# Optimization experiments

Hardware: AMD Instinct MI355X
Metric: run time of the kernel (lower is better)

Reference implementation:

```python
import jax, jax.numpy as jnp
import numpy as np

HID = 768        # config.hidden_size
MM_HID = 1024    # config.mmodal_hidden_size
N_Q = 64         # config.num_queries
WIN = 512        # config.window_size
LN_EPS = 1e-5


def _window_starts(m, n, w):
    # mirrors split_tensor's start-index logic (static, computed in numpy)
    step = max(1, (m - w) // (n - 1))
    starts = []
    for i in range(n):
        s = i * step
        if s + w > m:
            s = m - w
        starts.append(s)
    return np.asarray(starts, dtype=np.int32)


def layernorm(x, g, b):
    mu = jnp.mean(x, axis=-1, keepdims=True)
    var = jnp.var(x, axis=-1, keepdims=True)
    return (x - mu) * jax.lax.rsqrt(var + LN_EPS) * g + b


def setup_inputs() -> dict:
    key = jax.random.key(0)
    ks = jax.random.split(key, 12)
    b, m, li = 4, 8192, 77
    s = lambda fan_in: 1.0 / np.sqrt(fan_in)
    inp = {
        'x_mmodal': jax.random.normal(ks[0], (b, m, MM_HID), jnp.float32),
        'inst_feats': jax.random.normal(ks[1], (b, li, HID), jnp.float32),
        'queries': jax.random.normal(ks[2], (1, N_Q, HID), jnp.float32),
        'W_proj': jax.random.normal(ks[3], (HID, HID), jnp.float32) * s(HID),
        'b_proj': jnp.zeros((HID,), jnp.float32),
        'W_kv_inst': jax.random.normal(ks[4], (HID, 2 * HID), jnp.float32) * s(HID),
        'b_kv_inst': jnp.zeros((2 * HID,), jnp.float32),
        'W_out_inst': jax.random.normal(ks[5], (HID, HID), jnp.float32) * s(HID),
        'b_out_inst': jnp.zeros((HID,), jnp.float32),
        'W_kv_mm': jax.random.normal(ks[6], (MM_HID, 2 * HID), jnp.float32) * s(MM_HID),
        'b_kv_mm': jnp.zeros((2 * HID,), jnp.float32),
        'W_out_mm': jax.random.normal(ks[7], (HID, HID), jnp.float32) * s(HID),
        'b_out_mm': jnp.zeros((HID,), jnp.float32),
        'ln_g': jnp.ones((HID,), jnp.float32),
        'ln_b': jnp.zeros((HID,), jnp.float32),
    }
    return inp


def reference(x_mmodal, inst_feats, queries, W_proj, b_proj, W_kv_inst,
              b_kv_inst, W_out_inst, b_out_inst, W_kv_mm, b_kv_mm,
              W_out_mm, b_out_mm, ln_g, ln_b):
    b = x_mmodal.shape[0]
    scale = 1.0 / jnp.sqrt(jnp.asarray(HID, x_mmodal.dtype))

    # ---- dense cross-attention over instruction features ----
    inst = inst_feats @ W_proj + b_proj                      # (b, li, d)
    k, v = jnp.split(inst @ W_kv_inst + b_kv_inst, 2, axis=-1)
    k = layernorm(k, ln_g, ln_b)
    v = layernorm(v, ln_g, ln_b)
    q = jnp.broadcast_to(queries, (b, N_Q, HID))
    attn = jnp.einsum('bnd,bmd->bnm', q, k) * scale
    attn = jax.nn.softmax(attn, axis=-1)
    q = jnp.einsum('bnm,bmd->bnd', attn, v)
    q = layernorm(q @ W_out_inst + b_out_inst, ln_g, ln_b)

    # ---- swin-style overlapping windowed cross-attention over mmodal ----
    k, v = jnp.split(x_mmodal @ W_kv_mm + b_kv_mm, 2, axis=-1)
    k = layernorm(k, ln_g, ln_b)
    v = layernorm(v, ln_g, ln_b)
    m = k.shape[1]
    starts = _window_starts(m, N_Q, WIN)                     # (n,)
    idx = jnp.asarray(starts[:, None] + np.arange(WIN))      # (n, w)
    kw = k[:, idx]                                           # (b, n, w, d)
    vw = v[:, idx]                                           # (b, n, w, d)
    a = jnp.einsum('bnd,bnwd->bnw', q, kw) * scale
    a = jax.nn.softmax(a, axis=-1)
    out = jnp.einsum('bnw,bnwd->bnd', a, vw)
    out = layernorm(out @ W_out_mm + b_out_mm, ln_g, ln_b)
    return out
```

## Files before the change

kernel.cpp:

```cpp
#include <hip/hip_runtime.h>

#define HIDDEN 768
#define NQ 64
#define WINSZ 512
#define MSEQ 8192
#define BATCH 4
#define LI 77
#define MMHID 1024
#define LN_EPS 1e-5f
#define SCALE_QK 0.03608439182435161f

typedef __attribute__((ext_vector_type(8))) short short8v;
typedef __attribute__((ext_vector_type(4))) float f32x4;
typedef __attribute__((ext_vector_type(8))) unsigned short u16x8;

#define AS1 __attribute__((address_space(1)))
#define AS3 __attribute__((address_space(3)))

__device__ inline unsigned short f2bf(float f) {
    unsigned u = __float_as_uint(f);
    u += 0x7fffu + ((u >> 16) & 1u);
    return (unsigned short)(u >> 16);
}
__device__ inline float bf2f(unsigned short h) {
    return __uint_as_float(((unsigned)h) << 16);
}

__device__ inline void block_reduce2_256(float& s1, float& s2, float* sm) {
    #pragma unroll
    for (int o = 32; o; o >>= 1) { s1 += __shfl_down(s1, o); s2 += __shfl_down(s2, o); }
    int lane = threadIdx.x & 63, w = threadIdx.x >> 6;
    __syncthreads();
    if (lane == 0) { sm[w] = s1; sm[4 + w] = s2; }
    __syncthreads();
    s1 = sm[0] + sm[1] + sm[2] + sm[3];
    s2 = sm[4] + sm[5] + sm[6] + sm[7];
}

__global__ __launch_bounds__(256) void cvt_q_kernel(const float* __restrict__ q2,
                                                    const float* __restrict__ g,
                                                    const float* __restrict__ bb,
                                                    unsigned short* __restrict__ q2bf,
                                                    float* __restrict__ qgsum) {
    int blk = blockIdx.x;
    int b = blk >> 7, r = blk & 127;
    int t = threadIdx.x;
    __shared__ float sm[8];
    unsigned short* orow = q2bf + (size_t)blk * HIDDEN;
    if (r >= 64) {
        orow[t] = 0; orow[t + 256] = 0; orow[t + 512] = 0;
        return;
    }
    const float* qrow = q2 + ((size_t)(b * 64 + r)) * HIDDEN;
    float y0 = qrow[t], y1 = qrow[t + 256], y2 = qrow[t + 512];
    float s = y0 + y1 + y2, s2 = y0 * y0 + y1 * y1 + y2 * y2;
    block_reduce2_256(s, s2, sm);
    float mu = s * (1.f / 768.f);
    float var = s2 * (1.f / 768.f) - mu * mu;
    float inv = rsqrtf(var + LN_EPS);
    float qw0 = (y0 - mu) * inv * g[t]       + bb[t];
    float qw1 = (y1 - mu) * inv * g[t + 256] + bb[t + 256];
    float qw2 = (y2 - mu) * inv * g[t + 512] + bb[t + 512];
    float v0 = qw0 * g[t]       * SCALE_QK;
    float v1 = qw1 * g[t + 256] * SCALE_QK;
    float v2 = qw2 * g[t + 512] * SCALE_QK;
    orow[t] = f2bf(v0); orow[t + 256] = f2bf(v1); orow[t + 512] = f2bf(v2);
    float qs = v0 + v1 + v2, dummy = 0.f;
    block_reduce2_256(qs, dummy, sm);
    if (t == 0) qgsum[b * 64 + r] = qs;
}

struct PrepJobs {
    const float* W[5];
    unsigned short* Wt[5];
    int D[5];
    int C[5];
    const float* inst_in;
    unsigned short* inst_out;
    int n8_valid;
    int n8_total;
    const float* x_in;
    unsigned short* x_out;
    int n8x;
};
__global__ __launch_bounds__(256) void prep_kernel(PrepJobs tw) {
    int z = blockIdx.z;
    if (z >= 6) {
        int per_slice = (int)(gridDim.x * gridDim.y);
        int flat = blockIdx.y * gridDim.x + blockIdx.x;
        int i0 = ((z - 6) * per_slice + flat) * 256 + threadIdx.x;
        int stride = 2 * per_slice * 256;
        for (int i = i0; i < tw.n8x; i += stride) {
            const float4* p = (const float4*)(tw.x_in + (size_t)i * 8);
            float4 a = p[0], b = p[1];
            u16x8 o;
            o[0] = f2bf(a.x); o[1] = f2bf(a.y); o[2] = f2bf(a.z); o[3] = f2bf(a.w);
            o[4] = f2bf(b.x); o[5] = f2bf(b.y); o[6] = f2bf(b.z); o[7] = f2bf(b.w);
            *(u16x8*)(tw.x_out + (size_t)i * 8) = o;
        }
        return;
    }
    if (z == 5) {
        int flat = blockIdx.y * gridDim.x + blockIdx.x;
        int i = flat * 256 + threadIdx.x;
        if (i >= tw.n8_total) return;
        u16x8 o = {};
        if (i < tw.n8_valid) {
            const float4* p = (const float4*)(tw.inst_in + (size_t)i * 8);
            float4 a = p[0], b = p[1];
            o[0] = f2bf(a.x); o[1] = f2bf(a.y); o[2] = f2bf(a.z); o[3] = f2bf(a.w);
            o[4] = f2bf(b.x); o[5] = f2bf(b.y); o[6] = f2bf(b.z); o[7] = f2bf(b.w);
        }
        *(u16x8*)(tw.inst_out + (size_t)i * 8) = o;
        return;
    }
    int C = tw.C[z], D = tw.D[z];
    int n0 = blockIdx.x * 32, k0 = blockIdx.y * 32;
    if (n0 >= C || k0 >= D) return;
    const float* W = tw.W[z];
    unsigned short* Wt = tw.Wt[z];
    __shared__ float tile[32][33];
    int tx = threadIdx.x & 31, ty = (threadIdx.x >> 5);
    #pragma unroll
    for (int i = 0; i < 32; i += 8)
        tile[ty + i][tx] = W[(size_t)(k0 + ty + i) * C + n0 + tx];
    __syncthreads();
    #pragma unroll
    for (int i = 0; i < 32; i += 8)
        Wt[(size_t)(n0 + ty + i) * D + k0 + tx] = f2bf(tile[tx][ty + i]);
}

#define GM 32768
#define GN 1536
#define GK 1024

__global__ __launch_bounds__(512, 2) void gemm_kv256_kernel(const unsigned short* __restrict__ A,
                                                            const unsigned short* __restrict__ Bt,
                                                            const float* __restrict__ bias,
                                                            unsigned short* __restrict__ C) {
    extern __shared__ char smem[];
    unsigned short* sA = (unsigned short*)smem;
    unsigned short* sB = (unsigned short*)(smem + 65536);

    int nwg = gridDim.x;
    int bid = blockIdx.x;
    int wg = bid;
    if ((nwg & 7) == 0) { int cpx = nwg >> 3; wg = (bid & 7) * cpx + (bid >> 3); }
    int bm = wg / (GN / 256), bn = wg % (GN / 256);
    int row0 = bm * 256, col0 = bn * 256;

    int tid = threadIdx.x;
    int lane = tid & 63, wid = tid >> 6;
    int wm = wid >> 2, wn = wid & 3;

    f32x4 acc[8][4] = {};

    int rS[4], cS[4];
    #pragma unroll
    for (int i = 0; i < 4; i++) {
        int ch = wid * 4 + i;
        int r = ch * 8 + (lane >> 3);
        rS[i] = r;
        cS[i] = ((lane & 7) ^ (r & 7)) << 3;
    }

    auto STAGE = [&](int k0, int pbuf) {
        unsigned short* dA = sA + pbuf * 16384;
        unsigned short* dB = sB + pbuf * 16384;
        #pragma unroll
        for (int i = 0; i < 4; i++) {
            int ch = wid * 4 + i;
            const unsigned short* ga = A + (size_t)(row0 + rS[i]) * GK + k0 + cS[i];
            __builtin_amdgcn_global_load_lds((const AS1 unsigned int*)ga,
                                             (AS3 unsigned int*)&dA[ch * 512], 16, 0, 0);
            const unsigned short* gb = Bt + (size_t)(col0 + rS[i]) * GK + k0 + cS[i];
            __builtin_amdgcn_global_load_lds((const AS1 unsigned int*)gb,
                                             (AS3 unsigned int*)&dB[ch * 512], 16, 0, 0);
        }
    };

    STAGE(0, 0);
    __syncthreads();

    for (int kt = 0; kt < GK / 64; kt++) {
        int cur = kt & 1;
        if (kt < GK / 64 - 1) STAGE((kt + 1) * 64, cur ^ 1);

        const char* lA = (const char*)(sA + cur * 16384);
        const char* lB = (const char*)(sB + cur * 16384);

        short8v bfr[4][2];
        #pragma unroll
        for (int n = 0; n < 4; n++)
            #pragma unroll
            for (int kk = 0; kk < 2; kk++) {
                int r = wn * 64 + n * 16 + (lane & 15);
                int ko = (kk * 32 + ((lane >> 4) << 3)) * 2;
                bfr[n][kk] = *(const short8v*)(lB + r * 128 + (ko ^ ((r & 7) << 4)));
            }
        #pragma unroll
        for (int p = 0; p < 4; p++) {
            short8v afr[2][2];
            #pragma unroll
            for (int mf = 0; mf < 2; mf++)
                #pragma unroll
                for (int kk = 0; kk < 2; kk++) {
                    int r = wm * 128 + (p * 2 + mf) * 16 + (lane & 15);
                    int ko = (kk * 32 + ((lane >> 4) << 3)) * 2;
                    afr[mf][kk] = *(const short8v*)(lA + r * 128 + (ko ^ ((r & 7) << 4)));
                }
            __builtin_amdgcn_s_setprio(1);
            #pragma unroll
            for (int mf = 0; mf < 2; mf++)
                #pragma unroll
                for (int n = 0; n < 4; n++)
                    #pragma unroll
                    for (int kk = 0; kk < 2; kk++)
                        acc[p * 2 + mf][n] = __builtin_amdgcn_mfma_f32_16x16x32_bf16(
                            afr[mf][kk], bfr[n][kk], acc[p * 2 + mf][n], 0, 0, 0);
            __builtin_amdgcn_s_setprio(0);
        }
        __syncthreads();
    }

    int crow = (lane >> 4) * 4;
    int ccol = lane & 15;
    #pragma unroll
    for (int m = 0; m < 8; m++) {
        #pragma unroll
        for (int n = 0; n < 4; n++) {
            int gc = col0 + wn * 64 + n * 16 + ccol;
            float bv = bias[gc];
            #pragma unroll
            for (int j = 0; j < 4; j++) {
                int gr = row0 + wm * 128 + m * 16 + crow + j;
                C[(size_t)gr * GN + gc] = f2bf(acc[m][n][j] + bv);
            }
        }
    }
}

__global__ __launch_bounds__(256) void gemm_kv128_kernel(const unsigned short* __restrict__ A,
                                                         const unsigned short* __restrict__ Bt,
                                                         const float* __restrict__ bias,
                                                         unsigned short* __restrict__ C) {
    __shared__ unsigned short sA[128 * 64];
    __shared__ unsigned short sB[128 * 64];

    int nwg = gridDim.x;
    int bid = blockIdx.x;
    int wg = bid;
    if ((nwg & 7) == 0) { int cpx = nwg >> 3; wg = (bid & 7) * cpx + (bid >> 3); }
    int bm = wg / (GN / 128), bn = wg % (GN / 128);
    int row0 = bm * 128, col0 = bn * 128;

    int tid = threadIdx.x;
    int lane = tid & 63, wid = tid >> 6;
    int wr = wid >> 1, wc = wid & 1;

    f32x4 acc[4][4] = {};

    int rS[4], cS[4];
    #pragma unroll
    for (int i = 0; i < 4; i++) {
        int ch = wid * 4 + i;
        int r = ch * 8 + (lane >> 3);
        rS[i] = r;
        cS[i] = ((lane & 7) ^ (r & 7)) << 3;
    }

    for (int k0 = 0; k0 < GK; k0 += 64) {
        #pragma unroll
        for (int i = 0; i < 4; i++) {
            int ch = wid * 4 + i;
            const unsigned short* ga = A + (size_t)(row0 + rS[i]) * GK + k0 + cS[i];
            __builtin_amdgcn_global_load_lds((const AS1 unsigned int*)ga,
                                             (AS3 unsigned int*)&sA[ch * 512], 16, 0, 0);
            const unsigned short* gb = Bt + (size_t)(col0 + rS[i]) * GK + k0 + cS[i];
            __builtin_amdgcn_global_load_lds((const AS1 unsigned int*)gb,
                                             (AS3 unsigned int*)&sB[ch * 512], 16, 0, 0);
        }
        __syncthreads();

        #pragma unroll
        for (int kk = 0; kk < 64; kk += 32) {
            int ko = (kk + ((lane >> 4) << 3)) * 2;
            short8v af[4], bf[4];
            #pragma unroll
            for (int m = 0; m < 4; m++) {
                int r = wr * 64 + m * 16 + (lane & 15);
                int addr = r * 128 + (ko ^ ((r & 7) << 4));
                af[m] = *(const short8v*)((const char*)sA + addr);
            }
            #pragma unroll
            for (int n = 0; n < 4; n++) {
                int r = wc * 64 + n * 16 + (lane & 15);
                int addr = r * 128 + (ko ^ ((r & 7) << 4));
                bf[n] = *(const short8v*)((const char*)sB + addr);
            }
            #pragma unroll
            for (int m = 0; m < 4; m++)
                #pragma unroll
                for (int n = 0; n < 4; n++)
                    acc[m][n] = __builtin_amdgcn_mfma_f32_16x16x32_bf16(af[m], bf[n], acc[m][n], 0, 0, 0);
        }
        __syncthreads();
    }

    int crow = (lane >> 4) * 4;
    int ccol = lane & 15;
    #pragma unroll
    for (int m = 0; m < 4; m++) {
        #pragma unroll
        for (int n = 0; n < 4; n++) {
            int gc = col0 + wc * 64 + n * 16 + ccol;
            float bv = bias[gc];
            #pragma unroll
            for (int j = 0; j < 4; j++) {
                int gr = row0 + wr * 64 + m * 16 + crow + j;
                C[(size_t)gr * GN + gc] = f2bf(acc[m][n][j] + bv);
            }
        }
    }
}

__global__ __launch_bounds__(256) void stats_kernel(const unsigned short* __restrict__ kv,
                                                    float2* __restrict__ stats) {
    int rh = blockIdx.x;
    const unsigned short* p = kv + (size_t)rh * 768;
    int t = threadIdx.x;
    float x0 = bf2f(p[t]), x1 = bf2f(p[t + 256]), x2 = bf2f(p[t + 512]);
    float s = x0 + x1 + x2, s2 = x0 * x0 + x1 * x1 + x2 * x2;
    __shared__ float sm[8];
    block_reduce2_256(s, s2, sm);
    if (t == 0) {
        float mu = s * (1.f / 768.f);
        float var = s2 * (1.f / 768.f) - mu * mu;
        float inv = rsqrtf(var + LN_EPS);
        stats[rh] = make_float2(mu * inv, inv);
    }
}

template <int TK, bool OUT_BF16>
__global__ __launch_bounds__(256) void gemm_tile_kernel(const unsigned short* __restrict__ A,
                                                        const unsigned short* __restrict__ Bt,
                                                        const float* __restrict__ bias,
                                                        void* __restrict__ Cout, int N) {
    __shared__ unsigned short sA[128 * 64];
    __shared__ unsigned short sB[128 * 64];

    int row0 = blockIdx.x * 128, col0 = blockIdx.y * 128;
    int tid = threadIdx.x;
    int lane = tid & 63, wid = tid >> 6;
    int wr = wid >> 1, wc = wid & 1;

    f32x4 acc[4][4] = {};

    int rS[4], cS[4];
    #pragma unroll
    for (int i = 0; i < 4; i++) {
        int ch = wid * 4 + i;
        int r = ch * 8 + (lane >> 3);
        rS[i] = r;
        cS[i] = ((lane & 7) ^ (r & 7)) << 3;
    }

    for (int k0 = 0; k0 < TK; k0 += 64) {
        #pragma unroll
        for (int i = 0; i < 4; i++) {
            int ch = wid * 4 + i;
            const unsigned short* ga = A + (size_t)(row0 + rS[i]) * TK + k0 + cS[i];
            __builtin_amdgcn_global_load_lds((const AS1 unsigned int*)ga,
                                             (AS3 unsigned int*)&sA[ch * 512], 16, 0, 0);
            const unsigned short* gb = Bt + (size_t)(col0 + rS[i]) * TK + k0 + cS[i];
            __builtin_amdgcn_global_load_lds((const AS1 unsigned int*)gb,
                                             (AS3 unsigned int*)&sB[ch * 512], 16, 0, 0);
        }
        __syncthreads();

        #pragma unroll
        for (int kk = 0; kk < 64; kk += 32) {
            int ko = (kk + ((lane >> 4) << 3)) * 2;
            short8v af[4], bf[4];
            #pragma unroll
            for (int m = 0; m < 4; m++) {
                int r = wr * 64 + m * 16 + (lane & 15);
                int addr = r * 128 + (ko ^ ((r & 7) << 4));
                af[m] = *(const short8v*)((const char*)sA + addr);
            }
            #pragma unroll
            for (int n = 0; n < 4; n++) {
                int r = wc * 64 + n * 16 + (lane & 15);
                int addr = r * 128 + (ko ^ ((r & 7) << 4));
                bf[n] = *(const short8v*)((const char*)sB + addr);
            }
            #pragma unroll
            for (int m = 0; m < 4; m++)
                #pragma unroll
                for (int n = 0; n < 4; n++)
                    acc[m][n] = __builtin_amdgcn_mfma_f32_16x16x32_bf16(af[m], bf[n], acc[m][n], 0, 0, 0);
        }
        __syncthreads();
    }

    int crow = (lane >> 4) * 4;
    int ccol = lane & 15;
    #pragma unroll
    for (int m = 0; m < 4; m++) {
        #pragma unroll
        for (int n = 0; n < 4; n++) {
            int gc = col0 + wc * 64 + n * 16 + ccol;
            float bv = bias[gc];
            #pragma unroll
            for (int j = 0; j < 4; j++) {
                int gr = row0 + wr * 64 + m * 16 + crow + j;
                float v = acc[m][n][j] + bv;
                if (OUT_BF16) ((unsigned short*)Cout)[(size_t)gr * N + gc] = f2bf(v);
                else          ((float*)Cout)[(size_t)gr * N + gc] = v;
            }
        }
    }
}

__global__ __launch_bounds__(256) void gemm_scores_kernel(const unsigned short* __restrict__ Aall,
                                                          const unsigned short* __restrict__ kv,
                                                          float* __restrict__ scores) {
    __shared__ unsigned short sA[128 * 64];
    __shared__ unsigned short sB[128 * 64];

    int b = blockIdx.y;
    int col0 = blockIdx.x * 128;
    const unsigned short* A = Aall + (size_t)b * 128 * HIDDEN;
    const unsigned short* Bt = kv + (size_t)b * MSEQ * 1536;

    int tid = threadIdx.x;
    int lane = tid & 63, wid = tid >> 6;
    int wr = wid >> 1, wc = wid & 1;

    f32x4 acc[4][4] = {};

    int rS[4], cS[4];
    #pragma unroll
    for (int i = 0; i < 4; i++) {
        int ch = wid * 4 + i;
        int r = ch * 8 + (lane >> 3);
        rS[i] = r;
        cS[i] = ((lane & 7) ^ (r & 7)) << 3;
    }

    for (int k0 = 0; k0 < HIDDEN; k0 += 64) {
        #pragma unroll
        for (int i = 0; i < 4; i++) {
            int ch = wid * 4 + i;
            const unsigned short* ga = A + (size_t)rS[i] * HIDDEN + k0 + cS[i];
            __builtin_amdgcn_global_load_lds((const AS1 unsigned int*)ga,
                                             (AS3 unsigned int*)&sA[ch * 512], 16, 0, 0);
            const unsigned short* gb = Bt + (size_t)(col0 + rS[i]) * 1536 + k0 + cS[i];
            __builtin_amdgcn_global_load_lds((const AS1 unsigned int*)gb,
                                             (AS3 unsigned int*)&sB[ch * 512], 16, 0, 0);
        }
        __syncthreads();

        #pragma unroll
        for (int kk = 0; kk < 64; kk += 32) {
            int ko = (kk + ((lane >> 4) << 3)) * 2;
            short8v af[4], bf[4];
            #pragma unroll
            for (int m = 0; m < 4; m++) {
                int r = wr * 64 + m * 16 + (lane & 15);
                int addr = r * 128 + (ko ^ ((r & 7) << 4));
                af[m] = *(const short8v*)((const char*)sA + addr);
            }
            #pragma unroll
            for (int n = 0; n < 4; n++) {
                int r = wc * 64 + n * 16 + (lane & 15);
                int addr = r * 128 + (ko ^ ((r & 7) << 4));
                bf[n] = *(const short8v*)((const char*)sB + addr);
            }
            #pragma unroll
            for (int m = 0; m < 4; m++)
                #pragma unroll
                for (int n = 0; n < 4; n++)
                    acc[m][n] = __builtin_amdgcn_mfma_f32_16x16x32_bf16(af[m], bf[n], acc[m][n], 0, 0, 0);
        }
        __syncthreads();
    }

    int crow = (lane >> 4) * 4;
    int ccol = lane & 15;
    #pragma unroll
    for (int m = 0; m < 4; m++) {
        #pragma unroll
        for (int n = 0; n < 4; n++) {
            int gc = col0 + wc * 64 + n * 16 + ccol;
            #pragma unroll
            for (int j = 0; j < 4; j++) {
                int gr = wr * 64 + m * 16 + crow + j;
                if (gr < 64)
                    scores[((size_t)(b * 64 + gr)) * MSEQ + gc] = acc[m][n][j];
            }
        }
    }
}

__global__ __launch_bounds__(512) void win_softmax_kernel(const float* __restrict__ scores,
                                                          const float2* __restrict__ stats,
                                                          const float* __restrict__ qgsum,
                                                          unsigned short* __restrict__ P_abs,
                                                          float* __restrict__ s2out,
                                                          float* __restrict__ o_acc) {
    int bidx = blockIdx.x;
    int b = bidx >> 6, n = bidx & 63;
    int step = (MSEQ - WINSZ) / (NQ - 1);
    int s = n * step;
    if (s + WINSZ > MSEQ) s = MSEQ - WINSZ;

    __shared__ float sm[8];
    int t = threadIdx.x, lane = t & 63, w = t >> 6;

    float* oz = o_acc + ((size_t)(b * 64 + n)) * HIDDEN;
    oz[t] = 0.f;
    if (t < 256) oz[512 + t] = 0.f;

    int r_abs = s + t;
    size_t rowidx = (size_t)b * MSEQ + r_abs;
    float2 stk = stats[rowidx * 2 + 0];
    float qg = qgsum[b * 64 + n];
    float a = stk.y * scores[((size_t)(b * 64 + n)) * MSEQ + r_abs] - qg * stk.x;

    float m = a;
    #pragma unroll
    for (int o = 32; o; o >>= 1) m = fmaxf(m, __shfl_down(m, o));
    if (lane == 0) sm[w] = m;
    __syncthreads();
    m = sm[0];
    #pragma unroll
    for (int i = 1; i < 8; i++) m = fmaxf(m, sm[i]);
    float e = expf(a - m);
    float ssum = e;
    #pragma unroll
    for (int o = 32; o; o >>= 1) ssum += __shfl_down(ssum, o);
    __syncthreads();
    if (lane == 0) sm[w] = ssum;
    __syncthreads();
    ssum = 0;
    #pragma unroll
    for (int i = 0; i < 8; i++) ssum += sm[i];
    float p = e / ssum;

    float2 stv = stats[rowidx * 2 + 1];
    float pt = p * stv.y;
    float s2p = p * stv.x;
    #pragma unroll
    for (int o = 32; o; o >>= 1) s2p += __shfl_down(s2p, o);
    __syncthreads();
    if (lane == 0) sm[w] = s2p;
    __syncthreads();
    if (t == 0) {
        float s2 = 0;
        #pragma unroll
        for (int i = 0; i < 8; i++) s2 += sm[i];
        s2out[b * 64 + n] = s2;
    }

    unsigned short* prow = P_abs + ((size_t)(b * 64 + n)) * MSEQ;
    for (int pos = t; pos < MSEQ; pos += 512)
        if (pos < s || pos >= s + WINSZ) prow[pos] = 0;
    prow[r_abs] = f2bf(pt);
}

__global__ __launch_bounds__(768) void pv_chunk_kernel(const unsigned short* __restrict__ P_abs,
                                                       const unsigned short* __restrict__ kv,
                                                       float* __restrict__ out_acc) {
    int b = blockIdx.y;
    int r0 = blockIdx.x * 64;
    int t = threadIdx.x;

    int n_lo = (r0 >= 512) ? ((r0 - 512) / 121 + 1) : 0;
    int n_hi = (r0 + 63) / 121;
    if (n_hi > 63) n_hi = 63;

    __shared__ float pw[5][64];
    if (t < 5 * 64) {
        int ni = t >> 6, r = t & 63;
        int n = n_lo + ni;
        float v = 0.f;
        if (n <= n_hi)
            v = bf2f(P_abs[((size_t)(b * 64 + n)) * MSEQ + r0 + r]);
        pw[ni][r] = v;
    }
    __syncthreads();

    const unsigned short* vbase = kv + ((size_t)(b * MSEQ + r0)) * 1536 + 768;
    float acc[5] = {};
    #pragma unroll 8
    for (int r = 0; r < 64; ++r) {
        float v = bf2f(vbase[(size_t)r * 1536 + t]);
        #pragma unroll
        for (int ni = 0; ni < 5; ni++) acc[ni] = fmaf(v, pw[ni][r], acc[ni]);
    }
    #pragma unroll
    for (int ni = 0; ni < 5; ni++) {
        int n = n_lo + ni;
        if (n <= n_hi)
            atomicAdd(&out_acc[((size_t)(b * 64 + n)) * HIDDEN + t], acc[ni]);
    }
}

__global__ __launch_bounds__(256) void out_affine_kernel(const float* __restrict__ o_acc,
                                                         const float* __restrict__ s2,
                                                         const float* __restrict__ g,
                                                         const float* __restrict__ bb,
                                                         unsigned short* __restrict__ a_bf) {
    int i = blockIdx.x * 256 + threadIdx.x;
    if (i >= BATCH * NQ * HIDDEN) return;
    int n = i / HIDDEN, d = i - n * HIDDEN;
    a_bf[i] = f2bf(g[d] * (o_acc[i] - s2[n]) + bb[d]);
}

__global__ __launch_bounds__(256) void ln_f32_rows(float* __restrict__ base,
                                                   const float* __restrict__ g,
                                                   const float* __restrict__ b) {
    int rh = blockIdx.x;
    float* p = base + (size_t)rh * 768;
    int t = threadIdx.x;
    float x0 = p[t], x1 = p[t + 256], x2 = p[t + 512];
    float s = x0 + x1 + x2, s2 = x0 * x0 + x1 * x1 + x2 * x2;
    __shared__ float sm[8];
    block_reduce2_256(s, s2, sm);
    float mu = s * (1.f / 768.f);
    float var = s2 * (1.f / 768.f) - mu * mu;
    float inv = rsqrtf(var + LN_EPS);
    p[t]       = (x0 - mu) * inv * g[t]       + b[t];
    p[t + 256] = (x1 - mu) * inv * g[t + 256] + b[t + 256];
    p[t + 512] = (x2 - mu) * inv * g[t + 512] + b[t + 512];
}

__global__ __launch_bounds__(256) void attn_inst_kernel(const float* __restrict__ queries,
                                                        const float* __restrict__ kv,
                                                        const float* __restrict__ g,
                                                        const float* __restrict__ bb,
                                                        unsigned short* __restrict__ qatt) {
    int bidx = blockIdx.x;
    int b = bidx >> 6, n = bidx & 63;
    __shared__ float qg[HIDDEN];
    __shared__ float sc[LI], sc2[LI];
    __shared__ float2 stv[LI];
    __shared__ float sm[8];
    int t = threadIdx.x, lane = t & 63, w = t >> 6;
    const float* q = queries + (size_t)n * HIDDEN;
    float pgs = 0.f, pqb = 0.f;
    for (int d = t; d < HIDDEN; d += 256) {
        float qd = q[d], gg = g[d];
        qg[d] = qd * gg;
        pgs += qd * gg;
        pqb += qd * bb[d];
    }
    block_reduce2_256(pgs, pqb, sm);
    float qgs = pgs, qb = pqb;

    const float* kb = kv + (size_t)b * LI * 1536;
    for (int j = w; j < LI; j += 4) {
        const float* kr = kb + (size_t)j * 1536;
        const float* vr = kr + 768;
        float dotg = 0, sk = 0, s2k = 0, sv = 0, s2v = 0;
        #pragma unroll
        for (int i = 0; i < 12; i++) {
            int d = lane + i * 64;
            float kd = kr[d], vd = vr[d];
            dotg = fmaf(qg[d], kd, dotg);
            sk += kd; s2k = fmaf(kd, kd, s2k);
            sv += vd; s2v = fmaf(vd, vd, s2v);
        }
        #pragma unroll
        for (int o = 32; o; o >>= 1) {
            dotg += __shfl_down(dotg, o); sk += __shfl_down(sk, o); s2k += __shfl_down(s2k, o);
            sv += __shfl_down(sv, o); s2v += __shfl_down(s2v, o);
        }
        if (lane == 0) {
            float muk = sk * (1.f / 768.f);
            float invk = rsqrtf(s2k * (1.f / 768.f) - muk * muk + LN_EPS);
            sc[j] = SCALE_QK * (invk * dotg - muk * invk * qgs + qb);
            float muv = sv * (1.f / 768.f);
            float invv = rsqrtf(s2v * (1.f / 768.f) - muv * muv + LN_EPS);
            stv[j] = make_float2(muv * invv, invv);
        }
    }
    __syncthreads();
    float m = -1e30f;
    for (int j = 0; j < LI; j++) m = fmaxf(m, sc[j]);
    if (t < LI) sc2[t] = expf(sc[t] - m);
    __syncthreads();
    float s = 0;
    for (int j = 0; j < LI; j++) s += sc2[j];
    float invs = 1.f / s;
    float o0 = 0, o1 = 0, o2 = 0, s2sum = 0;
    for (int j = 0; j < LI; j++) {
        float p = sc2[j] * invs;
        float pt = p * stv[j].y;
        s2sum = fmaf(p, stv[j].x, s2sum);
        const float* vr = kb + (size_t)j * 1536 + 768;
        o0 = fmaf(pt, vr[t], o0);
        o1 = fmaf(pt, vr[t + 256], o1);
        o2 = fmaf(pt, vr[t + 512], o2);
    }
    unsigned short* orow = qatt + ((size_t)b * NQ + n) * HIDDEN;
    orow[t]       = f2bf(g[t]       * (o0 - s2sum) + bb[t]);
    orow[t + 256] = f2bf(g[t + 256] * (o1 - s2sum) + bb[t + 256]);
    orow[t + 512] = f2bf(g[t + 512] * (o2 - s2sum) + bb[t + 512]);
}

extern "C" void kernel_launch(void* const* d_in, const int* in_sizes, int n_in,
                              void* d_out, int out_size, void* d_ws, size_t ws_size,
                              hipStream_t stream) {
    (void)in_sizes; (void)n_in; (void)out_size; (void)ws_size;
    const float* x_mm    = (const float*)d_in[0];
    const float* instf   = (const float*)d_in[1];
    const float* queries = (const float*)d_in[2];
    const float* W_proj  = (const float*)d_in[3];
    const float* b_proj  = (const float*)d_in[4];
    const float* W_kvi   = (const float*)d_in[5];
    const float* b_kvi   = (const float*)d_in[6];
    const float* W_oi    = (const float*)d_in[7];
    const float* b_oi    = (const float*)d_in[8];
    const float* W_kvm   = (const float*)d_in[9];
    const float* b_kvm   = (const float*)d_in[10];
    const float* W_om    = (const float*)d_in[11];
    const float* b_om    = (const float*)d_in[12];
    const float* ln_g    = (const float*)d_in[13];
    const float* ln_b    = (const float*)d_in[14];
    float* out = (float*)d_out;

    char* ws = (char*)d_ws;
    size_t off = 0;
    auto carve = [&](size_t bytes) -> char* {
        char* p = ws + off;
        off += (bytes + 255) & ~(size_t)255;
        return p;
    };
    unsigned short* x_bf   = (unsigned short*)carve((size_t)BATCH * MSEQ * MMHID * 2);
    unsigned short* wtm_bf = (unsigned short*)carve((size_t)2 * HIDDEN * MMHID * 2);
    unsigned short* kv_mm  = (unsigned short*)carve((size_t)BATCH * MSEQ * 2 * HIDDEN * 2);
    unsigned short* wp_bf  = (unsigned short*)carve((size_t)768 * 768 * 2);
    unsigned short* wkvi_bf= (unsigned short*)carve((size_t)1536 * 768 * 2);
    unsigned short* woi_bf = (unsigned short*)carve((size_t)768 * 768 * 2);
    unsigned short* wom_bf = (unsigned short*)carve((size_t)768 * 768 * 2);
    unsigned short* a1_bf  = (unsigned short*)carve((size_t)384 * 768 * 2);
    unsigned short* inst_bf= (unsigned short*)carve((size_t)384 * 768 * 2);
    float*          kv_inst= (float*)carve((size_t)384 * 1536 * 4);
    unsigned short* qatt_bf= (unsigned short*)carve((size_t)256 * 768 * 2);
    float*          q2     = (float*)carve((size_t)256 * 768 * 4);
    unsigned short* q2bf   = (unsigned short*)carve((size_t)BATCH * 128 * 768 * 2);
    float*          scores = (float*)carve((size_t)BATCH * 64 * MSEQ * 4);
    unsigned short* P_abs  = (unsigned short*)carve((size_t)BATCH * 64 * MSEQ * 2);
    float*          o_acc  = (float*)carve((size_t)BATCH * 64 * 768 * 4);
    unsigned short* a_bf   = (unsigned short*)carve((size_t)256 * 768 * 2);
    float2*         stats  = (float2*)carve((size_t)BATCH * MSEQ * 2 * sizeof(float2));
    float*          qgsum  = (float*)carve((size_t)256 * 4);
    float*          s2     = (float*)carve((size_t)256 * 4);

    PrepJobs tw;
    tw.W[0] = W_kvm;  tw.Wt[0] = wtm_bf;  tw.D[0] = 1024; tw.C[0] = 1536;
    tw.W[1] = W_proj; tw.Wt[1] = wp_bf;   tw.D[1] = 768;  tw.C[1] = 768;
    tw.W[2] = W_kvi;  tw.Wt[2] = wkvi_bf; tw.D[2] = 768;  tw.C[2] = 1536;
    tw.W[3] = W_oi;   tw.Wt[3] = woi_bf;  tw.D[3] = 768;  tw.C[3] = 768;
    tw.W[4] = W_om;   tw.Wt[4] = wom_bf;  tw.D[4] = 768;  tw.C[4] = 768;
    tw.inst_in = instf; tw.inst_out = a1_bf;
    tw.n8_valid = BATCH * LI * 768 / 8; tw.n8_total = 384 * 768 / 8;
    tw.x_in = x_mm; tw.x_out = x_bf; tw.n8x = BATCH * MSEQ * MMHID / 8;
    prep_kernel<<<dim3(48, 32, 8), 256, 0, stream>>>(tw);

    hipError_t attr_ok = hipFuncSetAttribute((const void*)gemm_kv256_kernel,
                                             hipFuncAttributeMaxDynamicSharedMemorySize, 131072);
    if (attr_ok == hipSuccess) {
        gemm_kv256_kernel<<<(GM / 256) * (GN / 256), 512, 131072, stream>>>(x_bf, wtm_bf, b_kvm, kv_mm);
    } else {
        gemm_kv128_kernel<<<(GM / 128) * (GN / 128), 256, 0, stream>>>(x_bf, wtm_bf, b_kvm, kv_mm);
    }
    stats_kernel<<<BATCH * MSEQ * 2, 256, 0, stream>>>(kv_mm, stats);

    gemm_tile_kernel<768, true><<<dim3(3, 6), 256, 0, stream>>>(a1_bf, wp_bf, b_proj, inst_bf, 768);
    gemm_tile_kernel<768, false><<<dim3(3, 12), 256, 0, stream>>>(inst_bf, wkvi_bf, b_kvi, kv_inst, 1536);
    attn_inst_kernel<<<BATCH * NQ, 256, 0, stream>>>(queries, kv_inst, ln_g, ln_b, qatt_bf);
    gemm_tile_kernel<768, false><<<dim3(2, 6), 256, 0, stream>>>(qatt_bf, woi_bf, b_oi, q2, 768);

    cvt_q_kernel<<<BATCH * 128, 256, 0, stream>>>(q2, ln_g, ln_b, q2bf, qgsum);
    gemm_scores_kernel<<<dim3(MSEQ / 128, BATCH), 256, 0, stream>>>(q2bf, kv_mm, scores);
    win_softmax_kernel<<<BATCH * NQ, 512, 0, stream>>>(scores, stats, qgsum, P_abs, s2, o_acc);
    pv_chunk_kernel<<<dim3(MSEQ / 64, BATCH), 768, 0, stream>>>(P_abs, kv_mm, o_acc);
    out_affine_kernel<<<(BATCH * NQ * HIDDEN + 255) / 256, 256, 0, stream>>>(o_acc, s2, ln_g, ln_b, a_bf);

    gemm_tile_kernel<768, false><<<dim3(2, 6), 256, 0, stream>>>(a_bf, wom_bf, b_om, out, 768);
    ln_f32_rows<<<BATCH * NQ, 256, 0, stream>>>(out, ln_g, ln_b);
}
```

Measured before the change: 321.2 us.

## Fuse layernorm row statistics into KV GEMM epilogue

Computes per-row sum and sum of squares of the KV projection inside the GEMM epilogue, reducing across lanes and in shared memory via atomics. Each tile writes partial stats, and a small finalize kernel combines the three column tiles per half into mean/inv-std. This removes the separate stats pass that re-read the full bf16 KV buffer. The trade-offs are extra epilogue work, and stats computed from unrounded fp32 values using a one-pass variance.

```diff
diff --git a/kernel.cpp b/kernel.cpp
--- a/kernel.cpp
+++ b/kernel.cpp
@@ -137,7 +137,8 @@
 __global__ __launch_bounds__(512, 2) void gemm_kv256_kernel(const unsigned short* __restrict__ A,
                                                             const unsigned short* __restrict__ Bt,
                                                             const float* __restrict__ bias,
-                                                            unsigned short* __restrict__ C) {
+                                                            unsigned short* __restrict__ C,
+                                                            float2* __restrict__ stat_s) {
     extern __shared__ char smem[];
     unsigned short* sA = (unsigned short*)smem;
     unsigned short* sB = (unsigned short*)(smem + 65536);
@@ -223,10 +224,17 @@
         __syncthreads();
     }
 
+    float2* rowpart = (float2*)smem;
+    if (tid < 256) rowpart[tid] = make_float2(0.f, 0.f);
+    __syncthreads();
+
     int crow = (lane >> 4) * 4;
     int ccol = lane & 15;
+    int half = (col0 >= 768) ? 1 : 0;
+    int tilei = (col0 - half * 768) >> 8;
     #pragma unroll
     for (int m = 0; m < 8; m++) {
+        float rs[4] = {}, rq[4] = {};
         #pragma unroll
         for (int n = 0; n < 4; n++) {
             int gc = col0 + wn * 64 + n * 16 + ccol;
@@ -234,10 +242,41 @@
             #pragma unroll
             for (int j = 0; j < 4; j++) {
                 int gr = row0 + wm * 128 + m * 16 + crow + j;
-                C[(size_t)gr * GN + gc] = f2bf(acc[m][n][j] + bv);
-            }
-        }
-    }
+                float v = acc[m][n][j] + bv;
+                C[(size_t)gr * GN + gc] = f2bf(v);
+                rs[j] += v; rq[j] += v * v;
+            }
+        }
+        #pragma unroll
+        for (int j = 0; j < 4; j++) {
+            float s_ = rs[j], q_ = rq[j];
+            #pragma unroll
+            for (int o = 8; o; o >>= 1) { s_ += __shfl_xor(s_, o); q_ += __shfl_xor(q_, o); }
+            if (ccol == 0) {
+                int lr = wm * 128 + m * 16 + crow + j;
+                atomicAdd(&rowpart[lr].x, s_);
+                atomicAdd(&rowpart[lr].y, q_);
+            }
+        }
+    }
+    __syncthreads();
+    if (tid < 256) {
+        int gr = row0 + tid;
+        stat_s[((size_t)gr * 2 + half) * 3 + tilei] = rowpart[tid];
+    }
+}
+
+__global__ __launch_bounds__(256) void stats_fin_kernel(const float2* __restrict__ part,
+                                                        float2* __restrict__ stats, int n) {
+    int i = blockIdx.x * 256 + threadIdx.x;
+    if (i >= n) return;
+    float2 a0 = part[(size_t)i * 3], a1 = part[(size_t)i * 3 + 1], a2 = part[(size_t)i * 3 + 2];
+    float sx = a0.x + a1.x + a2.x;
+    float sq = a0.y + a1.y + a2.y;
+    float mu = sx * (1.f / 768.f);
+    float var = sq * (1.f / 768.f) - mu * mu;
+    float inv = rsqrtf(var + LN_EPS);
+    stats[i] = make_float2(mu * inv, inv);
 }
 
 __global__ __launch_bounds__(256) void gemm_kv128_kernel(const unsigned short* __restrict__ A,
@@ -756,6 +795,7 @@
     float*          o_acc  = (float*)carve((size_t)BATCH * 64 * 768 * 4);
     unsigned short* a_bf   = (unsigned short*)carve((size_t)256 * 768 * 2);
     float2*         stats  = (float2*)carve((size_t)BATCH * MSEQ * 2 * sizeof(float2));
+    float2*         stat_s = (float2*)carve((size_t)BATCH * MSEQ * 2 * 3 * sizeof(float2));
     float*          qgsum  = (float*)carve((size_t)256 * 4);
     float*          s2     = (float*)carve((size_t)256 * 4);
 
@@ -773,11 +813,12 @@
     hipError_t attr_ok = hipFuncSetAttribute((const void*)gemm_kv256_kernel,
                                              hipFuncAttributeMaxDynamicSharedMemorySize, 131072);
     if (attr_ok == hipSuccess) {
-        gemm_kv256_kernel<<<(GM / 256) * (GN / 256), 512, 131072, stream>>>(x_bf, wtm_bf, b_kvm, kv_mm);
+        gemm_kv256_kernel<<<(GM / 256) * (GN / 256), 512, 131072, stream>>>(x_bf, wtm_bf, b_kvm, kv_mm, stat_s);
+        stats_fin_kernel<<<(BATCH * MSEQ * 2 + 255) / 256, 256, 0, stream>>>(stat_s, stats, BATCH * MSEQ * 2);
     } else {
         gemm_kv128_kernel<<<(GM / 128) * (GN / 128), 256, 0, stream>>>(x_bf, wtm_bf, b_kvm, kv_mm);
-    }
-    stats_kernel<<<BATCH * MSEQ * 2, 256, 0, stream>>>(kv_mm, stats);
+        stats_kernel<<<BATCH * MSEQ * 2, 256, 0, stream>>>(kv_mm, stats);
+    }
 
     gemm_tile_kernel<768, true><<<dim3(3, 6), 256, 0, stream>>>(a1_bf, wp_bf, b_proj, inst_bf, 768);
     gemm_tile_kernel<768, false><<<dim3(3, 12), 256, 0, stream>>>(inst_bf, wkvi_bf, b_kvi, kv_inst, 1536);
```

After: 302.2 us. -5.9%, faster.
